# Kernel tuning notes

Hardware: AMD Instinct MI355X
Metric: run time of the kernel (lower is better)

The kernel has to match this reference:

```python
import jax, jax.numpy as jnp
import numpy as np

CHUNK = 32


def l2norm(x):
    return x * jax.lax.rsqrt(jnp.sum(x * x, -1, keepdims=True) + 1e-6)


def causal_dwconv(x, w):
    # x: (b, l, C), w: (C, 1, k) -- depthwise causal 1D conv (left pad k-1)
    k = w.shape[-1]
    xt = jnp.transpose(x, (0, 2, 1))
    xt = jnp.pad(xt, ((0, 0), (0, 0), (k - 1, 0)))
    y = jax.lax.conv_general_dilated(xt, w, (1,), 'VALID',
                                     dimension_numbers=('NCH', 'OIH', 'NCH'),
                                     feature_group_count=xt.shape[1])
    return jnp.transpose(y, (0, 2, 1))


def delta_rule_chunkwise(q, k, v, beta):
    # q,k: (b,h,L,dk), v: (b,h,L,dv), beta: (b,h,L). L must be divisible by CHUNK.
    b, h, L, dk = q.shape
    dv = v.shape[-1]
    n = L // CHUNK
    q = l2norm(q)
    k = l2norm(k)
    v = v * beta[..., None]
    kb = k * beta[..., None]
    resh = lambda t: t.reshape(b, h, n, CHUNK, t.shape[-1])
    q, k, v, kb = (resh(t) for t in (q, k, v, kb))
    strict = jnp.tril(jnp.ones((CHUNK, CHUNK), bool), -1)
    A = jnp.where(strict, -(kb @ jnp.swapaxes(k, -1, -2)), 0.0)
    eye = jnp.eye(CHUNK, dtype=A.dtype)
    # UT transform: the sequential forward-substitution loop computes T = (I - A)^{-1}
    T = jax.scipy.linalg.solve_triangular(eye - A, jnp.broadcast_to(eye, A.shape), lower=True)
    u = T @ v
    w = T @ kb
    incl = jnp.tril(jnp.ones((CHUNK, CHUNK), bool))  # lower incl. diag

    def step(S, xs):
        q_i, k_i, u_i, w_i = xs
        attn = jnp.where(incl, q_i @ jnp.swapaxes(k_i, -1, -2), 0.0)
        u_hat = u_i - w_i @ S
        o_i = q_i @ S + attn @ u_hat
        return S + jnp.swapaxes(k_i, -1, -2) @ u_hat, o_i

    xs = tuple(jnp.moveaxis(t, 2, 0) for t in (q, k, u, w))
    S0 = jnp.zeros((b, h, dk, dv), q.dtype)
    S, o = jax.lax.scan(step, S0, xs)
    o = jnp.moveaxis(o, 0, 2).reshape(b, h, L, dv)
    return o, S


def branch_stats(x):
    # per-head stats over the feature dim: mean, std(ddof=1), mean|x|, L2 norm
    m = jnp.mean(x, -1, keepdims=True)
    s = jnp.std(x, -1, keepdims=True, ddof=1)
    a = jnp.mean(jnp.abs(x), -1, keepdims=True)
    l = jnp.sqrt(jnp.sum(x * x, -1, keepdims=True))
    return jnp.concatenate([m, s, a, l], -1)


def reference(hidden_states, q_w, k_w, v_w, b_w, qc_w, kc_w, vc_w,
              fir_w1, fir_w3, fir_w7, fir_w31,
              mlp_w1, mlp_b1, mlp_w2, mlp_b2, gate_log_temp, onorm_w, o_w):
    B, L, D = hidden_states.shape
    H = gate_log_temp.shape[0]
    dk = q_w.shape[1] // H
    dv = v_w.shape[1] // H
    # projections + causal short conv + silu
    q = jax.nn.silu(causal_dwconv(hidden_states @ q_w, qc_w))
    k = jax.nn.silu(causal_dwconv(hidden_states @ k_w, kc_w))
    v = jax.nn.silu(causal_dwconv(hidden_states @ v_w, vc_w))
    q = q.reshape(B, L, H, dk)
    k = k.reshape(B, L, H, dk)
    v_direct = v.reshape(B, L, H, dv)
    beta = jax.nn.sigmoid(hidden_states @ b_w)  # (B,L,H)
    delta_out, _ = delta_rule_chunkwise(
        jnp.transpose(q, (0, 2, 1, 3)), jnp.transpose(k, (0, 2, 1, 3)),
        jnp.transpose(v_direct, (0, 2, 1, 3)), jnp.transpose(beta, (0, 2, 1)))
    delta_out = jnp.transpose(delta_out, (0, 2, 1, 3))  # (B,L,H,dv)
    # multi-scale depthwise FIR branches on v
    v_flat = v_direct.reshape(B, L, H * dv)
    firs = [causal_dwconv(v_flat, w).reshape(B, L, H, dv)
            for w in (fir_w1, fir_w3, fir_w7, fir_w31)]
    branches = firs + [delta_out, v_direct]  # num_streams = 6
    S = len(branches)
    stats = jnp.concatenate([branch_stats(x) for x in branches], -1)  # (B,L,H,S*4)
    gate_in = jnp.concatenate([hidden_states, stats.reshape(B, L, H * S * 4)], -1)
    hgate = jax.nn.gelu(gate_in @ mlp_w1 + mlp_b1, approximate=False)
    logits = (hgate @ mlp_w2 + mlp_b2).reshape(B, L, H, S)
    temp = jax.nn.softplus(gate_log_temp) + 0.5  # min_gate_temp = 0.5
    weights = jax.nn.softmax(logits / temp[None, None, :, None], axis=-1)
    fused = sum(weights[..., i, None] * br for i, br in enumerate(branches))
    # RMSNorm over head_v_dim (eps=1e-5)
    fused = fused * jax.lax.rsqrt(jnp.mean(fused * fused, -1, keepdims=True) + 1e-5) * onorm_w
    return fused.reshape(B, L, H * dv) @ o_w


def setup_inputs() -> dict:
    key = jax.random.key(0)
    B, L, D, H = 2, 2048, 1024, 4
    dk = dv = D // H
    S = 6
    ks = iter(jax.random.split(key, 32))
    nrm = lambda shape, s=0.02: jax.random.normal(next(ks), shape, jnp.float32) * s

    def fir(kw):
        # delta init (last tap = 1) plus small noise
        base = jnp.zeros((H * dv, 1, kw), jnp.float32).at[:, 0, -1].set(1.0)
        return base + nrm((H * dv, 1, kw))

    gate_in_dim = D + S * 4 * H  # 1120
    hgd = D * 2 // 2             # 1024
    b2 = np.zeros(H * S, np.float32)
    for h in range(H):
        b2[h * S + S - 1] = 2.0  # value_bias_init on direct-value stream
    return {
        'hidden_states': jax.random.normal(next(ks), (B, L, D), jnp.float32),
        'q_w': nrm((D, D)), 'k_w': nrm((D, D)), 'v_w': nrm((D, D)),
        'b_w': nrm((D, H)),
        'qc_w': nrm((D, 1, 4), 0.3), 'kc_w': nrm((D, 1, 4), 0.3), 'vc_w': nrm((D, 1, 4), 0.3),
        'fir_w1': fir(1), 'fir_w3': fir(3), 'fir_w7': fir(7), 'fir_w31': fir(31),
        'mlp_w1': nrm((gate_in_dim, hgd)), 'mlp_b1': jnp.zeros((hgd,), jnp.float32),
        'mlp_w2': nrm((hgd, H * S)), 'mlp_b2': jnp.asarray(b2),
        'gate_log_temp': jnp.zeros((H,), jnp.float32),
        'onorm_w': jnp.ones((dv,), jnp.float32),
        'o_w': nrm((D, D)),
    }
```

## Files before the change

### kernel.cpp

```cpp
#include <hip/hip_runtime.h>
#include <hip/hip_bf16.h>
#include <math.h>

#define B_ 2
#define L_ 2048
#define D_ 1024
#define H_ 4
#define NC 64

typedef unsigned short ushort_t;
typedef __bf16 bf16x8 __attribute__((ext_vector_type(8)));
typedef float f32x4 __attribute__((ext_vector_type(4)));
typedef ushort_t u16x8 __attribute__((ext_vector_type(8)));

__device__ __forceinline__ ushort_t f2bs(float f) {
    __hip_bfloat16 h = __float2bfloat16(f);
    ushort_t u;
    __builtin_memcpy(&u, &h, 2);
    return u;
}

__device__ __forceinline__ float wred(float v) {
    v += __shfl_down(v, 32);
    v += __shfl_down(v, 16);
    v += __shfl_down(v, 8);
    v += __shfl_down(v, 4);
    v += __shfl_down(v, 2);
    v += __shfl_down(v, 1);
    return v;
}

__device__ __forceinline__ void gload16(const void* g, void* l) {
    __builtin_amdgcn_global_load_lds((const __attribute__((address_space(1))) void*)g,
                                     (__attribute__((address_space(3))) void*)l, 16, 0, 0);
}

__global__ __launch_bounds__(256) void tcast_k(const float* __restrict__ W,
                                               ushort_t* __restrict__ WT, int K, int N) {
    __shared__ float tile[32 * 33];
    const int k0 = blockIdx.y << 5, n0 = blockIdx.x << 5;
    for (int e = threadIdx.x; e < 1024; e += 256)
        tile[(e >> 5) * 33 + (e & 31)] = W[(size_t)(k0 + (e >> 5)) * N + n0 + (e & 31)];
    __syncthreads();
    for (int e = threadIdx.x; e < 1024; e += 256)
        WT[(size_t)(n0 + (e >> 5)) * K + k0 + (e & 31)] = f2bs(tile[(e & 31) * 33 + (e >> 5)]);
}

__global__ __launch_bounds__(256) void cast_k(const float* __restrict__ x,
                                              ushort_t* __restrict__ y) {
    const int i = blockIdx.x * 256 + threadIdx.x;
    const float4 v = *(const float4*)&x[(size_t)i * 4];
    ushort4 p;
    p.x = f2bs(v.x); p.y = f2bs(v.y); p.z = f2bs(v.z); p.w = f2bs(v.w);
    *(ushort4*)&y[(size_t)i * 4] = p;
}

template <int ACT>
__global__ __launch_bounds__(256) void gemm_bf(const ushort_t* __restrict__ A,
                                               const ushort_t* __restrict__ Bt,
                                               const float* __restrict__ bias,
                                               float* __restrict__ C,
                                               int M, int N, int K) {
    __shared__ ushort_t As[128 * 32];
    __shared__ ushort_t Bs[128 * 32];
    const int t = threadIdx.x;
    const int wv = t >> 6, l = t & 63;
    const int m0 = blockIdx.y << 7, n0 = blockIdx.x << 7;
    const int wm = wv & 1, wn = wv >> 1;
    const int q4 = l >> 4, c16 = l & 15;
    f32x4 acc[4][4];
#pragma unroll
    for (int i = 0; i < 4; ++i)
#pragma unroll
        for (int j = 0; j < 4; ++j) {
            f32x4 z = {0.f, 0.f, 0.f, 0.f};
            acc[i][j] = z;
        }
    const int srow = (l >> 2);
    const int scol = (l & 3) << 3;
    for (int k0 = 0; k0 < K; k0 += 32) {
        __syncthreads();
#pragma unroll
        for (int si = 0; si < 2; ++si) {
            const int s = wv * 2 + si;
            gload16(&A[(size_t)(m0 + s * 16 + srow) * K + k0 + scol], &As[s * 512]);
            gload16(&Bt[(size_t)(n0 + s * 16 + srow) * K + k0 + scol], &Bs[s * 512]);
        }
        __syncthreads();
        bf16x8 af[4], bff[4];
#pragma unroll
        for (int mi = 0; mi < 4; ++mi)
            af[mi] = *(const bf16x8*)&As[(wm * 64 + mi * 16 + c16) * 32 + q4 * 8];
#pragma unroll
        for (int ni = 0; ni < 4; ++ni)
            bff[ni] = *(const bf16x8*)&Bs[(wn * 64 + ni * 16 + c16) * 32 + q4 * 8];
#pragma unroll
        for (int mi = 0; mi < 4; ++mi)
#pragma unroll
            for (int ni = 0; ni < 4; ++ni)
                acc[mi][ni] = __builtin_amdgcn_mfma_f32_16x16x32_bf16(af[mi], bff[ni],
                                                                     acc[mi][ni], 0, 0, 0);
    }
#pragma unroll
    for (int mi = 0; mi < 4; ++mi)
#pragma unroll
        for (int ni = 0; ni < 4; ++ni)
#pragma unroll
            for (int r = 0; r < 4; ++r) {
                const int row = m0 + wm * 64 + mi * 16 + q4 * 4 + r;
                const int col = n0 + wn * 64 + ni * 16 + c16;
                float v = acc[mi][ni][r];
                if (ACT == 1) {
                    v += bias[col];
                    v = 0.5f * v * (1.0f + erff(v * 0.70710678118654752f));
                }
                C[(size_t)row * N + col] = v;
            }
}

template <int DO_NORM, int EMIT_F32, int EMIT_BF>
__global__ __launch_bounds__(256) void convql_k(const float* __restrict__ X,
                                                const float* __restrict__ cw,
                                                float* __restrict__ Y,
                                                ushort_t* __restrict__ Ybf) {
    __shared__ float xs[35 * 256];
    const int bid = blockIdx.x;
    const int h = bid & 3, lt = (bid >> 2) & 63, b = bid >> 8;
    const int t = threadIdx.x;
    const int l0 = lt << 5;
    const int cg = (h << 8) | t;
    for (int e = t; e < 35 * 256; e += 256) {
        const int r = e >> 8, c = e & 255;
        const int gl = l0 + r - 3;
        xs[e] = (gl >= 0) ? X[((size_t)(b * L_) + gl) * 3072 + (h << 8) + c] : 0.f;
    }
    const float w0 = cw[cg * 4 + 0], w1 = cw[cg * 4 + 1];
    const float w2 = cw[cg * 4 + 2], w3 = cw[cg * 4 + 3];
    __syncthreads();
    float yr[32];
#pragma unroll
    for (int l = 0; l < 32; ++l) {
        const float a = xs[(l + 0) * 256 + t] * w0 + xs[(l + 1) * 256 + t] * w1 +
                        xs[(l + 2) * 256 + t] * w2 + xs[(l + 3) * 256 + t] * w3;
        yr[l] = a / (1.f + expf(-a));
    }
    if (DO_NORM) {
        __syncthreads();
#pragma unroll
        for (int l = 0; l < 32; ++l) xs[l * 256 + t] = yr[l];
        __syncthreads();
        const int wv = t >> 6, lane = t & 63;
#pragma unroll
        for (int ri = 0; ri < 8; ++ri) {
            const int r = wv * 8 + ri;
            float4 v = *(float4*)&xs[r * 256 + lane * 4];
            float ss = v.x * v.x + v.y * v.y + v.z * v.z + v.w * v.w;
            ss = wred(ss);
            ss = __shfl(ss, 0);
            const float s = rsqrtf(ss + 1e-6f);
            v.x *= s; v.y *= s; v.z *= s; v.w *= s;
            const size_t go = ((size_t)(b * L_) + l0 + r) * 1024 + (h << 8) + lane * 4;
            if (EMIT_F32) *(float4*)&Y[go] = v;
            if (EMIT_BF) {
                ushort4 p;
                p.x = f2bs(v.x); p.y = f2bs(v.y); p.z = f2bs(v.z); p.w = f2bs(v.w);
                *(ushort4*)&Ybf[go] = p;
            }
        }
    } else {
#pragma unroll
        for (int l = 0; l < 32; ++l)
            if (EMIT_F32) Y[((size_t)(b * L_) + l0 + l) * 1024 + cg] = yr[l];
    }
}

__global__ __launch_bounds__(256) void fir_k(const float* __restrict__ V,
                                             const float* __restrict__ w1w,
                                             const float* __restrict__ w3w,
                                             const float* __restrict__ w7w,
                                             const float* __restrict__ w31w,
                                             float* __restrict__ o1,
                                             float* __restrict__ o3,
                                             float* __restrict__ o7,
                                             float* __restrict__ o31) {
    __shared__ float xs[62 * 256];
    const int bid = blockIdx.x;
    const int h = bid & 3, lt = (bid >> 2) & 63, b = bid >> 8;
    const int t = threadIdx.x;
    const int l0 = lt << 5;
    const int cg = (h << 8) | t;
    for (int e = t; e < 62 * 256; e += 256) {
        const int r = e >> 8, c = e & 255;
        const int gl = l0 + r - 30;
        xs[e] = (gl >= 0) ? V[((size_t)(b * L_) + gl) * 1024 + (h << 8) + c] : 0.f;
    }
    float lw31[31], lw7[7], lw3[3];
#pragma unroll
    for (int j = 0; j < 31; ++j) lw31[j] = w31w[cg * 31 + j];
#pragma unroll
    for (int j = 0; j < 7; ++j) lw7[j] = w7w[cg * 7 + j];
#pragma unroll
    for (int j = 0; j < 3; ++j) lw3[j] = w3w[cg * 3 + j];
    const float lw1 = w1w[cg];
    __syncthreads();
    for (int l = 0; l < 32; ++l) {
        float a31 = 0.f, a7 = 0.f, a3 = 0.f, v = 0.f;
#pragma unroll
        for (int j = 0; j < 31; ++j) {
            v = xs[(l + j) * 256 + t];
            a31 += v * lw31[j];
            if (j >= 24) a7 += v * lw7[j - 24];
            if (j >= 28) a3 += v * lw3[j - 28];
        }
        const size_t go = ((size_t)(b * L_) + l0 + l) * 1024 + cg;
        o31[go] = a31;
        o7[go] = a7;
        o3[go] = a3;
        o1[go] = v * lw1;
    }
}

__global__ __launch_bounds__(64) void beta_k(const float* __restrict__ hs,
                                             const float* __restrict__ bw,
                                             float* __restrict__ beta,
                                             ushort_t* __restrict__ gin) {
    const int row = blockIdx.x;
    const int lane = threadIdx.x;
    float a0 = 0, a1 = 0, a2 = 0, a3 = 0;
    const float* hp = hs + (size_t)row * D_;
    ushort_t* gp = gin + (size_t)row * 1120;
    for (int c = lane; c < D_; c += 64) {
        const float x = hp[c];
        gp[c] = f2bs(x);
        a0 += x * bw[c * 4 + 0];
        a1 += x * bw[c * 4 + 1];
        a2 += x * bw[c * 4 + 2];
        a3 += x * bw[c * 4 + 3];
    }
    a0 = wred(a0); a1 = wred(a1); a2 = wred(a2); a3 = wred(a3);
    if (lane == 0) {
        float* o = beta + (size_t)row * 4;
        o[0] = 1.f / (1.f + expf(-a0));
        o[1] = 1.f / (1.f + expf(-a1));
        o[2] = 1.f / (1.f + expf(-a2));
        o[3] = 1.f / (1.f + expf(-a3));
    }
}

__global__ __launch_bounds__(256) void prep2_k(const ushort_t* __restrict__ qbf,
                                               const ushort_t* __restrict__ kbf,
                                               const float* __restrict__ vg,
                                               const float* __restrict__ beta,
                                               ushort_t* __restrict__ qfr,
                                               ushort_t* __restrict__ wfr,
                                               float* __restrict__ ufr,
                                               ushort_t* __restrict__ atfr,
                                               ushort_t* __restrict__ ktfr) {
    __shared__ ushort_t k_lds[32 * 264];
    __shared__ ushort_t kT_lds[256 * 32];
    __shared__ ushort_t vT_lds[256 * 32];
    __shared__ float Am[32 * 33];
    __shared__ float Tm[32 * 33];
    __shared__ ushort_t Tb[32 * 40];
    __shared__ ushort_t at_s[32 * 40];
    __shared__ float beta_s[32];
    const int bid = blockIdx.x;
    const int bh = bid >> 6, ci = bid & 63;
    const int b = bh >> 2, h = bh & 3;
    const int t = threadIdx.x;
    const int wv = t >> 6, lane = t & 63;
    const int mi = wv & 1, ni = wv >> 1;
    const int l16 = lane & 15, quad = lane >> 4;
    const size_t cb = (size_t)bid;
    const size_t grow = ((size_t)(b * L_ + ci * 32)) * 1024 + (h << 8);
    const f32x4 z4 = {0.f, 0.f, 0.f, 0.f};

    if (t < 32) beta_s[t] = beta[(size_t)(b * L_ + ci * 32 + t) * 4 + h];
#pragma unroll
    for (int j = 0; j < 4; ++j) {
        const int idx = j * 2048 + t * 8, r = idx >> 8, c = idx & 255;
        *(u16x8*)&k_lds[r * 264 + c] = *(const u16x8*)&kbf[grow + (size_t)r * 1024 + c];
    }
#pragma unroll
    for (int j = 0; j < 8; ++j) {
        const int e = j * 1024 + t * 4, r = e >> 8, c = e & 255;
        const float4 v4 = *(const float4*)&vg[grow + (size_t)r * 1024 + c];
        const float vv[4] = {v4.x, v4.y, v4.z, v4.w};
#pragma unroll
        for (int x = 0; x < 4; ++x) {
            const int cc = c + x;
            const int sp = (r >> 3) ^ ((cc >> 1) & 3);
            vT_lds[cc * 32 + sp * 8 + (r & 7)] = f2bs(vv[x]);
        }
    }
    f32x4 g = z4, atv = z4;
#pragma unroll
    for (int s = 0; s < 8; ++s) {
        const bf16x8 a =
            *(const bf16x8*)&kbf[grow + (size_t)(mi * 16 + l16) * 1024 + s * 32 + (quad << 3)];
        const bf16x8 bb =
            *(const bf16x8*)&kbf[grow + (size_t)(ni * 16 + l16) * 1024 + s * 32 + (quad << 3)];
        const bf16x8 qa =
            *(const bf16x8*)&qbf[grow + (size_t)(mi * 16 + l16) * 1024 + s * 32 + (quad << 3)];
        g = __builtin_amdgcn_mfma_f32_16x16x32_bf16(a, bb, g, 0, 0, 0);
        atv = __builtin_amdgcn_mfma_f32_16x16x32_bf16(qa, bb, atv, 0, 0, 0);
        if (ni == 0) *(bf16x8*)&qfr[((cb * 2 + mi) * 8 + s) * 512 + lane * 8] = qa;
    }
    __syncthreads();
#pragma unroll
    for (int r = 0; r < 4; ++r) {
        const int row = mi * 16 + (quad << 2) + r;
        const int col = ni * 16 + l16;
        Am[row * 33 + col] = (col < row) ? -beta_s[row] * g[r] : 0.f;
        Tm[row * 33 + col] = (row == col) ? 1.f : 0.f;
        at_s[row * 40 + col] = (col <= row) ? f2bs(atv[r]) : (ushort_t)0;
    }
#pragma unroll
    for (int j = 0; j < 8; ++j) {
        const int e = j * 1024 + t * 4, r = e >> 8, c = e & 255;
#pragma unroll
        for (int x = 0; x < 4; ++x) {
            const int cc = c + x;
            const int sp = (r >> 3) ^ ((cc >> 1) & 3);
            kT_lds[cc * 32 + sp * 8 + (r & 7)] = k_lds[r * 264 + cc];
        }
    }
    __syncthreads();
    if (wv < 2) {
        const u16x8 av = *(const u16x8*)&at_s[(wv * 16 + l16) * 40 + (quad << 3)];
        *(u16x8*)&atfr[(cb * 2 + wv) * 512 + lane * 8] = av;
    }
#pragma unroll
    for (int j2 = 0; j2 < 4; ++j2) {
        const int tc = wv * 4 + j2;
        const int c = tc * 16 + l16;
        const int sp = quad ^ ((c >> 1) & 3);
        *(u16x8*)&ktfr[(cb * 16 + tc) * 512 + lane * 8] = *(const u16x8*)&kT_lds[c * 32 + sp * 8];
    }
    for (int i = 1; i < 32; ++i) {
        if (t < 32) {
            float s = 0.f;
            for (int j = 0; j < i; ++j) s += Am[i * 33 + j] * Tm[j * 33 + t];
            Tm[i * 33 + t] += s;
        }
        __syncthreads();
    }
#pragma unroll
    for (int j = 0; j < 4; ++j) {
        const int e = j * 256 + t, i = e >> 5, jj = e & 31;
        Tb[i * 40 + jj] = f2bs(Tm[i * 33 + jj] * beta_s[jj]);
    }
    __syncthreads();
    const bf16x8 tf = *(const bf16x8*)&Tb[(mi * 16 + l16) * 40 + (quad << 3)];
#pragma unroll
    for (int j = 0; j < 8; ++j) {
        const int nt = ni * 8 + j;
        const int d = (nt << 4) + l16;
        const int sp = quad ^ ((d >> 1) & 3);
        const bf16x8 kb = *(const bf16x8*)&kT_lds[d * 32 + (sp << 3)];
        const bf16x8 vb = *(const bf16x8*)&vT_lds[d * 32 + (sp << 3)];
        const f32x4 wacc = __builtin_amdgcn_mfma_f32_16x16x32_bf16(tf, kb, z4, 0, 0, 0);
        const f32x4 uacc = __builtin_amdgcn_mfma_f32_16x16x32_bf16(tf, vb, z4, 0, 0, 0);
        *(float4*)&ufr[((cb * 16 + nt) * 2 + mi) * 256 + lane * 4] =
            make_float4(uacc[0], uacc[1], uacc[2], uacc[3]);
#pragma unroll
        for (int r = 0; r < 4; ++r) {
            const int row = mi * 16 + (quad << 2) + r;
            k_lds[row * 264 + d] = f2bs(wacc[r]);
        }
    }
    __syncthreads();
    if (wv < 2) {
#pragma unroll
        for (int s = 0; s < 8; ++s) {
            const u16x8 wv8 = *(const u16x8*)&k_lds[(wv * 16 + l16) * 264 + s * 32 + (quad << 3)];
            *(u16x8*)&wfr[((cb * 2 + wv) * 8 + s) * 512 + lane * 8] = wv8;
        }
    }
}

__global__ __launch_bounds__(64, 1) void scan7_k(const ushort_t* __restrict__ qfr,
                                                 const ushort_t* __restrict__ wfr,
                                                 const float* __restrict__ ufr,
                                                 const ushort_t* __restrict__ atfr,
                                                 const ushort_t* __restrict__ ktfr,
                                                 float* __restrict__ dlt) {
    __shared__ ushort_t qstg[2][16 * 512];
    __shared__ ushort_t wstg[2][16 * 512];
    __shared__ ushort_t atstg[2][2 * 512];
    __shared__ float ustg[2][2 * 256];
    __shared__ ushort_t Sm[8 * 512];
    __shared__ ushort_t uhL[512];
    const int l = threadIdx.x;
    const int q = l >> 4, c = l & 15;
    const int bh = blockIdx.x & 7, tile = blockIdx.x >> 3;
    const int b = bh >> 2, h = bh & 3;

    const int4 z16 = {0, 0, 0, 0};
#pragma unroll
    for (int e = 0; e < 8; ++e) *(int4*)&Sm[(e * 64 + l) * 8] = z16;

    f32x4 Sacc[16];
#pragma unroll
    for (int tc = 0; tc < 16; ++tc) {
        f32x4 z = {0.f, 0.f, 0.f, 0.f};
        Sacc[tc] = z;
    }

    auto stage = [&](int ci, int p) {
        const size_t cb = (size_t)(bh * NC + ci);
        const ushort_t* qsrc = qfr + cb * (16 * 512);
        const ushort_t* wsrc = wfr + cb * (16 * 512);
#pragma unroll
        for (int f = 0; f < 16; ++f) gload16(&qsrc[f * 512 + l * 8], &qstg[p][f * 512]);
#pragma unroll
        for (int f = 0; f < 16; ++f) gload16(&wsrc[f * 512 + l * 8], &wstg[p][f * 512]);
#pragma unroll
        for (int hf = 0; hf < 2; ++hf)
            gload16(&atfr[(cb * 2 + hf) * 512 + l * 8], &atstg[p][hf * 512]);
#pragma unroll
        for (int hf = 0; hf < 2; ++hf)
            gload16(&ufr[((cb * 16 + tile) * 2 + hf) * 256 + l * 4], &ustg[p][hf * 256]);
    };

    stage(0, 0);
    asm volatile("s_waitcnt vmcnt(0)" ::: "memory");
    __builtin_amdgcn_sched_barrier(0);

    for (int ci = 0; ci < NC; ++ci) {
        const int p = ci & 1;
        asm volatile("s_waitcnt vmcnt(8)" ::: "memory");
        __builtin_amdgcn_sched_barrier(0);
        const size_t cb = (size_t)(bh * NC + ci);
        bf16x8 ktf[16];
        const ushort_t* ksrc = ktfr + cb * (16 * 512);
#pragma unroll
        for (int tc = 0; tc < 16; ++tc)
            ktf[tc] = *(const bf16x8*)&ksrc[tc * 512 + l * 8];
        if (ci + 1 < NC) stage(ci + 1, p ^ 1);

        f32x4 aw0[2], aw1[2], oq0[2], oq1[2];
#pragma unroll
        for (int hf = 0; hf < 2; ++hf) {
            f32x4 z = {0.f, 0.f, 0.f, 0.f};
            aw0[hf] = z; aw1[hf] = z; oq0[hf] = z; oq1[hf] = z;
        }
#pragma unroll
        for (int s = 0; s < 8; ++s) {
            const bf16x8 Sb = *(const bf16x8*)&Sm[(s * 64 + l) * 8];
            const bf16x8 w0 = *(const bf16x8*)&wstg[p][(0 * 8 + s) * 512 + l * 8];
            const bf16x8 w1 = *(const bf16x8*)&wstg[p][(1 * 8 + s) * 512 + l * 8];
            const bf16x8 q0 = *(const bf16x8*)&qstg[p][(0 * 8 + s) * 512 + l * 8];
            const bf16x8 q1 = *(const bf16x8*)&qstg[p][(1 * 8 + s) * 512 + l * 8];
            if (s & 1) {
                aw1[0] = __builtin_amdgcn_mfma_f32_16x16x32_bf16(w0, Sb, aw1[0], 0, 0, 0);
                aw1[1] = __builtin_amdgcn_mfma_f32_16x16x32_bf16(w1, Sb, aw1[1], 0, 0, 0);
                oq1[0] = __builtin_amdgcn_mfma_f32_16x16x32_bf16(q0, Sb, oq1[0], 0, 0, 0);
                oq1[1] = __builtin_amdgcn_mfma_f32_16x16x32_bf16(q1, Sb, oq1[1], 0, 0, 0);
            } else {
                aw0[0] = __builtin_amdgcn_mfma_f32_16x16x32_bf16(w0, Sb, aw0[0], 0, 0, 0);
                aw0[1] = __builtin_amdgcn_mfma_f32_16x16x32_bf16(w1, Sb, aw0[1], 0, 0, 0);
                oq0[0] = __builtin_amdgcn_mfma_f32_16x16x32_bf16(q0, Sb, oq0[0], 0, 0, 0);
                oq0[1] = __builtin_amdgcn_mfma_f32_16x16x32_bf16(q1, Sb, oq0[1], 0, 0, 0);
            }
        }
#pragma unroll
        for (int hf = 0; hf < 2; ++hf) {
            const float4 uv = *(const float4*)&ustg[p][hf * 256 + l * 4];
            ushort4 up;
            up.x = f2bs(uv.x - aw0[hf][0] - aw1[hf][0]);
            up.y = f2bs(uv.y - aw0[hf][1] - aw1[hf][1]);
            up.z = f2bs(uv.z - aw0[hf][2] - aw1[hf][2]);
            up.w = f2bs(uv.w - aw0[hf][3] - aw1[hf][3]);
            *(ushort4*)&uhL[((2 * hf + (q >> 1)) * 16 + c) * 8 + (q & 1) * 4] = up;
        }
        const bf16x8 uhB = *(const bf16x8*)&uhL[l * 8];
#pragma unroll
        for (int tc = 0; tc < 16; ++tc) {
            Sacc[tc] = __builtin_amdgcn_mfma_f32_16x16x32_bf16(ktf[tc], uhB, Sacc[tc], 0, 0, 0);
            ushort4 pk;
            pk.x = f2bs(Sacc[tc][0]);
            pk.y = f2bs(Sacc[tc][1]);
            pk.z = f2bs(Sacc[tc][2]);
            pk.w = f2bs(Sacc[tc][3]);
            *(ushort4*)&Sm[(((tc >> 1) * 64) + ((tc & 1) * 2 + (q >> 1)) * 16 + c) * 8 +
                           (q & 1) * 4] = pk;
        }
        const bf16x8 at0 = *(const bf16x8*)&atstg[p][0 * 512 + l * 8];
        const bf16x8 at1 = *(const bf16x8*)&atstg[p][1 * 512 + l * 8];
        oq0[0] = __builtin_amdgcn_mfma_f32_16x16x32_bf16(at0, uhB, oq0[0], 0, 0, 0);
        oq0[1] = __builtin_amdgcn_mfma_f32_16x16x32_bf16(at1, uhB, oq0[1], 0, 0, 0);
        const size_t gbase = ((size_t)(b * L_ + ci * 32)) * 1024 + (h << 8) + (tile << 4) + c;
#pragma unroll
        for (int hf = 0; hf < 2; ++hf)
#pragma unroll
            for (int r = 0; r < 4; ++r)
                dlt[gbase + (size_t)(hf * 16 + (q << 2) + r) * 1024] = oq0[hf][r] + oq1[hf][r];
    }
}

__global__ __launch_bounds__(64) void stats_k(const float* __restrict__ f1,
                                              const float* __restrict__ f3,
                                              const float* __restrict__ f7,
                                              const float* __restrict__ f31,
                                              const float* __restrict__ dl,
                                              const float* __restrict__ vv,
                                              ushort_t* __restrict__ gin) {
    const int row = blockIdx.x;
    const int lane = threadIdx.x;
    const float* ptrs[6] = {f1, f3, f7, f31, dl, vv};
    const size_t base = (size_t)row * 256;
    ushort_t* gp = gin + (size_t)(row >> 2) * 1120 + 1024 + (row & 3) * 24;
    for (int br = 0; br < 6; ++br) {
        const float4 x = *(const float4*)&ptrs[br][base + lane * 4];
        float s1 = x.x + x.y + x.z + x.w;
        float s2 = x.x * x.x + x.y * x.y + x.z * x.z + x.w * x.w;
        float sa = fabsf(x.x) + fabsf(x.y) + fabsf(x.z) + fabsf(x.w);
        s1 = wred(s1); s2 = wred(s2); sa = wred(sa);
        if (lane == 0) {
            const float m = s1 / 256.f;
            float var = (s2 - 256.f * m * m) / 255.f;
            if (var < 0.f) var = 0.f;
            gp[br * 4 + 0] = f2bs(m);
            gp[br * 4 + 1] = f2bs(sqrtf(var));
            gp[br * 4 + 2] = f2bs(sa / 256.f);
            gp[br * 4 + 3] = f2bs(sqrtf(s2));
        }
    }
}

__global__ __launch_bounds__(256) void wts_k(const float* __restrict__ hg,
                                             const float* __restrict__ w2,
                                             const float* __restrict__ b2,
                                             const float* __restrict__ glt,
                                             float* __restrict__ wts) {
    const int row = blockIdx.x;
    const int h = threadIdx.x >> 6, lane = threadIdx.x & 63;
    float hv[16];
    const float* hp = hg + (size_t)row * 1024;
#pragma unroll
    for (int ii = 0; ii < 16; ++ii) hv[ii] = hp[lane + 64 * ii];
    float lg[6];
#pragma unroll
    for (int s = 0; s < 6; ++s) {
        const int j = h * 6 + s;
        float acc = 0.f;
#pragma unroll
        for (int ii = 0; ii < 16; ++ii) acc += hv[ii] * w2[(size_t)(lane + 64 * ii) * 24 + j];
        lg[s] = wred(acc);
    }
    if (lane == 0) {
        const float temp = log1pf(expf(glt[h])) + 0.5f;
        float mx = -1e30f;
#pragma unroll
        for (int s = 0; s < 6; ++s) {
            lg[s] = (lg[s] + b2[h * 6 + s]) / temp;
            mx = fmaxf(mx, lg[s]);
        }
        float se = 0.f;
#pragma unroll
        for (int s = 0; s < 6; ++s) {
            lg[s] = expf(lg[s] - mx);
            se += lg[s];
        }
        float* o = &wts[(size_t)row * 24 + h * 6];
        const float inv = 1.f / se;
#pragma unroll
        for (int s = 0; s < 6; ++s) o[s] = lg[s] * inv;
    }
}

__global__ __launch_bounds__(1024) void fuse_k(const float* __restrict__ f1,
                                               const float* __restrict__ f3,
                                               const float* __restrict__ f7,
                                               const float* __restrict__ f31,
                                               const float* __restrict__ dl,
                                               const float* __restrict__ vv,
                                               const float* __restrict__ wts,
                                               const float* __restrict__ onw,
                                               ushort_t* __restrict__ fused) {
    __shared__ float wloc[24];
    __shared__ float psum[16];
    const int row = blockIdx.x, t = threadIdx.x;
    if (t < 24) wloc[t] = wts[(size_t)row * 24 + t];
    __syncthreads();
    const int h = t >> 8, dd = t & 255;
    const size_t idx = (size_t)row * 1024 + t;
    const float* ptrs[6] = {f1, f3, f7, f31, dl, vv};
    float f = 0.f;
#pragma unroll
    for (int br = 0; br < 6; ++br) f += wloc[h * 6 + br] * ptrs[br][idx];
    float ss = wred(f * f);
    const int wave = t >> 6;
    if ((t & 63) == 0) psum[wave] = ss;
    __syncthreads();
    const float tot = psum[h * 4 + 0] + psum[h * 4 + 1] + psum[h * 4 + 2] + psum[h * 4 + 3];
    const float scale = rsqrtf(tot / 256.f + 1e-5f);
    fused[idx] = f2bs(f * scale * onw[dd]);
}

extern "C" void kernel_launch(void* const* d_in, const int* in_sizes, int n_in,
                              void* d_out, int out_size, void* d_ws, size_t ws_size,
                              hipStream_t stream) {
    const float* hs   = (const float*)d_in[0];
    const float* q_w  = (const float*)d_in[1];
    const float* k_w  = (const float*)d_in[2];
    const float* v_w  = (const float*)d_in[3];
    const float* b_w  = (const float*)d_in[4];
    const float* qc_w = (const float*)d_in[5];
    const float* kc_w = (const float*)d_in[6];
    const float* vc_w = (const float*)d_in[7];
    const float* f1w  = (const float*)d_in[8];
    const float* f3w  = (const float*)d_in[9];
    const float* f7w  = (const float*)d_in[10];
    const float* f31w = (const float*)d_in[11];
    const float* w1   = (const float*)d_in[12];
    const float* b1   = (const float*)d_in[13];
    const float* w2   = (const float*)d_in[14];
    const float* b2   = (const float*)d_in[15];
    const float* glt  = (const float*)d_in[16];
    const float* onw  = (const float*)d_in[17];
    const float* o_w  = (const float*)d_in[18];
    float* out = (float*)d_out;

    const size_t SZ = (size_t)B_ * L_ * D_;
    float* qlin = (float*)d_ws;
    float* klin = qlin + SZ;
    float* vlin = klin + SZ;
    float* qbuf = vlin + SZ;
    float* kbuf = qbuf + SZ;
    float* vbuf = kbuf + SZ;
    float* f31b = vbuf + SZ;
    float* wb   = f31b + SZ;
    float* ub   = wb + SZ;
    float* dlt  = ub + SZ;
    float* beta = dlt + SZ;
    float* attn = beta + (size_t)B_ * L_ * H_;
    float* f1b = qlin;
    float* f3b = klin;
    float* f7b = vlin;
    float* hgate = kbuf;
    float* qkv = qlin;
    float* wts = attn + (size_t)B_ * H_ * NC * 1024;

    ushort_t* hs_bf = (ushort_t*)dlt;
    ushort_t* qwT = (ushort_t*)f31b;
    ushort_t* kwT = (ushort_t*)f31b + 1048576;
    ushort_t* vwT = (ushort_t*)f31b + 2097152;
    ushort_t* qbf = (ushort_t*)f31b + 3145728;
    ushort_t* kbf = (ushort_t*)kbuf;
    ushort_t* gin_bf = (ushort_t*)qbuf;
    ushort_t* w1T = (ushort_t*)(wb + 2359296);
    ushort_t* owT = (ushort_t*)ub;
    ushort_t* fused_bf = (ushort_t*)kbuf;
    ushort_t* ktfr = (ushort_t*)klin;
    ushort_t* qfr = (ushort_t*)klin + SZ;
    ushort_t* wfr = (ushort_t*)wb;
    float* ufr = ub;
    ushort_t* atfr = (ushort_t*)attn;

    const int M = B_ * L_;

    tcast_k<<<dim3(32, 32), 256, 0, stream>>>(q_w, qwT, 1024, 1024);
    tcast_k<<<dim3(32, 32), 256, 0, stream>>>(k_w, kwT, 1024, 1024);
    tcast_k<<<dim3(32, 32), 256, 0, stream>>>(v_w, vwT, 1024, 1024);
    cast_k<<<4096, 256, 0, stream>>>(hs, hs_bf);
    gemm_bf<0><<<dim3(24, 32), 256, 0, stream>>>(hs_bf, qwT, nullptr, qkv, M, 3072, 1024);
    beta_k<<<M, 64, 0, stream>>>(hs, b_w, beta, gin_bf);
    convql_k<1, 0, 1><<<512, 256, 0, stream>>>(qkv + 0,    qc_w, nullptr, qbf);
    convql_k<1, 0, 1><<<512, 256, 0, stream>>>(qkv + 1024, kc_w, nullptr, kbf);
    convql_k<0, 1, 0><<<512, 256, 0, stream>>>(qkv + 2048, vc_w, vbuf, nullptr);
    prep2_k<<<B_ * H_ * NC, 256, 0, stream>>>(qbf, kbf, vbuf, beta, qfr, wfr, ufr, atfr, ktfr);
    scan7_k<<<128, 64, 0, stream>>>(qfr, wfr, ufr, atfr, ktfr, dlt);
    fir_k<<<512, 256, 0, stream>>>(vbuf, f1w, f3w, f7w, f31w, f1b, f3b, f7b, f31b);
    stats_k<<<M * H_, 64, 0, stream>>>(f1b, f3b, f7b, f31b, dlt, vbuf, gin_bf);
    tcast_k<<<dim3(32, 35), 256, 0, stream>>>(w1, w1T, 1120, 1024);
    gemm_bf<1><<<dim3(8, 32), 256, 0, stream>>>(gin_bf, w1T, b1, hgate, M, 1024, 1120);
    wts_k<<<M, 256, 0, stream>>>(hgate, w2, b2, glt, wts);
    fuse_k<<<M, 1024, 0, stream>>>(f1b, f3b, f7b, f31b, dlt, vbuf, wts, onw, fused_bf);
    tcast_k<<<dim3(32, 32), 256, 0, stream>>>(o_w, owT, 1024, 1024);
    gemm_bf<0><<<dim3(8, 32), 256, 0, stream>>>(fused_bf, owT, nullptr, out, M, 1024, 1024);
}
```

Measured before the change: 585.0 us.

## Keep scan state in registers by re-laying MFMA fragments to avoid LDS round-trips

The prep kernel now writes the q, attn, k^T and w fragments in a permuted k-order, with each lane's 8 elements drawn as two 4-element halves 16 apart. This lets the MFMA output of S (bf16-packed) and u_hat feed straight back as B operands from registers, so the scan no longer stages S and u_hat through shared memory between MFMAs. The scan also prefetches the next chunk's k^T fragments into double-buffered registers and unrolls two chunks per iteration, and it drops the split even/odd accumulators. The cost is much higher register pressure in a serial, one-wave-per-block kernel, plus a strict requirement that the permuted layout stays consistent across both kernels.

```diff
diff --git a/kernel.cpp b/kernel.cpp
--- a/kernel.cpp
+++ b/kernel.cpp
@@ -12,6 +12,8 @@
 typedef __bf16 bf16x8 __attribute__((ext_vector_type(8)));
 typedef float f32x4 __attribute__((ext_vector_type(4)));
 typedef ushort_t u16x8 __attribute__((ext_vector_type(8)));
+typedef short s16x8 __attribute__((ext_vector_type(8)));
+typedef short s16x4 __attribute__((ext_vector_type(4)));
 
 __device__ __forceinline__ ushort_t f2bs(float f) {
     __hip_bfloat16 h = __float2bfloat16(f);
@@ -33,6 +35,16 @@
 __device__ __forceinline__ void gload16(const void* g, void* l) {
     __builtin_amdgcn_global_load_lds((const __attribute__((address_space(1))) void*)g,
                                      (__attribute__((address_space(3))) void*)l, 16, 0, 0);
+}
+
+__device__ __forceinline__ s16x4 pack4(float a, float b, float c, float d) {
+    ushort4 u;
+    u.x = f2bs(a); u.y = f2bs(b); u.z = f2bs(c); u.w = f2bs(d);
+    return __builtin_bit_cast(s16x4, u);
+}
+__device__ __forceinline__ bf16x8 cat8(s16x4 lo, s16x4 hi) {
+    s16x8 r = __builtin_shufflevector(lo, hi, 0, 1, 2, 3, 4, 5, 6, 7);
+    return __builtin_bit_cast(bf16x8, r);
 }
 
 __global__ __launch_bounds__(256) void tcast_k(const float* __restrict__ W,
@@ -304,7 +316,14 @@
             *(const bf16x8*)&qbf[grow + (size_t)(mi * 16 + l16) * 1024 + s * 32 + (quad << 3)];
         g = __builtin_amdgcn_mfma_f32_16x16x32_bf16(a, bb, g, 0, 0, 0);
         atv = __builtin_amdgcn_mfma_f32_16x16x32_bf16(qa, bb, atv, 0, 0, 0);
-        if (ni == 0) *(bf16x8*)&qfr[((cb * 2 + mi) * 8 + s) * 512 + lane * 8] = qa;
+        if (ni == 0) {
+            const size_t ga = grow + (size_t)(mi * 16 + l16) * 1024 + s * 32 + (quad << 2);
+            const ushort4 q0 = *(const ushort4*)&qbf[ga];
+            const ushort4 q1 = *(const ushort4*)&qbf[ga + 16];
+            ushort_t* qd = &qfr[((cb * 2 + mi) * 8 + s) * 512 + lane * 8];
+            *(ushort4*)qd = q0;
+            *(ushort4*)(qd + 4) = q1;
+        }
     }
     __syncthreads();
 #pragma unroll
@@ -327,15 +346,24 @@
     }
     __syncthreads();
     if (wv < 2) {
-        const u16x8 av = *(const u16x8*)&at_s[(wv * 16 + l16) * 40 + (quad << 3)];
-        *(u16x8*)&atfr[(cb * 2 + wv) * 512 + lane * 8] = av;
+        const int ra = (wv * 16 + l16) * 40 + (quad << 2);
+        const ushort4 a0 = *(const ushort4*)&at_s[ra];
+        const ushort4 a1 = *(const ushort4*)&at_s[ra + 16];
+        ushort_t* ad = &atfr[(cb * 2 + wv) * 512 + lane * 8];
+        *(ushort4*)ad = a0;
+        *(ushort4*)(ad + 4) = a1;
     }
 #pragma unroll
     for (int j2 = 0; j2 < 4; ++j2) {
         const int tc = wv * 4 + j2;
-        const int c = tc * 16 + l16;
-        const int sp = quad ^ ((c >> 1) & 3);
-        *(u16x8*)&ktfr[(cb * 16 + tc) * 512 + lane * 8] = *(const u16x8*)&kT_lds[c * 32 + sp * 8];
+        const int d = tc * 16 + l16;
+        const int x = (d >> 1) & 3;
+        const int base = d * 32 + ((quad & 1) << 2);
+        const ushort4 k0 = *(const ushort4*)&kT_lds[base + ((((quad >> 1) + 0) ^ x) << 3)];
+        const ushort4 k1 = *(const ushort4*)&kT_lds[base + ((((quad >> 1) + 2) ^ x) << 3)];
+        ushort_t* kd = &ktfr[(cb * 16 + tc) * 512 + lane * 8];
+        *(ushort4*)kd = k0;
+        *(ushort4*)(kd + 4) = k1;
     }
     for (int i = 1; i < 32; ++i) {
         if (t < 32) {
@@ -372,14 +400,18 @@
     __syncthreads();
     if (wv < 2) {
 #pragma unroll
-        for (int s = 0; s < 8; ++s) {
-            const u16x8 wv8 = *(const u16x8*)&k_lds[(wv * 16 + l16) * 264 + s * 32 + (quad << 3)];
-            *(u16x8*)&wfr[((cb * 2 + wv) * 8 + s) * 512 + lane * 8] = wv8;
-        }
-    }
-}
-
-__global__ __launch_bounds__(64, 1) void scan7_k(const ushort_t* __restrict__ qfr,
+        for (int sp = 0; sp < 8; ++sp) {
+            const int rb = (wv * 16 + l16) * 264 + sp * 32 + (quad << 2);
+            const ushort4 w0 = *(const ushort4*)&k_lds[rb];
+            const ushort4 w1 = *(const ushort4*)&k_lds[rb + 16];
+            ushort_t* wd = &wfr[((cb * 2 + wv) * 8 + sp) * 512 + lane * 8];
+            *(ushort4*)wd = w0;
+            *(ushort4*)(wd + 4) = w1;
+        }
+    }
+}
+
+__global__ __launch_bounds__(64, 1) void scan9_k(const ushort_t* __restrict__ qfr,
                                                  const ushort_t* __restrict__ wfr,
                                                  const float* __restrict__ ufr,
                                                  const ushort_t* __restrict__ atfr,
@@ -389,23 +421,21 @@
     __shared__ ushort_t wstg[2][16 * 512];
     __shared__ ushort_t atstg[2][2 * 512];
     __shared__ float ustg[2][2 * 256];
-    __shared__ ushort_t Sm[8 * 512];
-    __shared__ ushort_t uhL[512];
     const int l = threadIdx.x;
-    const int q = l >> 4, c = l & 15;
+    const int qd = l >> 4, c = l & 15;
     const int bh = blockIdx.x & 7, tile = blockIdx.x >> 3;
     const int b = bh >> 2, h = bh & 3;
 
-    const int4 z16 = {0, 0, 0, 0};
-#pragma unroll
-    for (int e = 0; e < 8; ++e) *(int4*)&Sm[(e * 64 + l) * 8] = z16;
-
     f32x4 Sacc[16];
+    s16x4 SB[16];
 #pragma unroll
     for (int tc = 0; tc < 16; ++tc) {
         f32x4 z = {0.f, 0.f, 0.f, 0.f};
         Sacc[tc] = z;
-    }
+        s16x4 zs = {0, 0, 0, 0};
+        SB[tc] = zs;
+    }
+    s16x8 ktA[16], ktB[16];
 
     auto stage = [&](int ci, int p) {
         const size_t cb = (size_t)(bh * NC + ci);
@@ -423,80 +453,68 @@
             gload16(&ufr[((cb * 16 + tile) * 2 + hf) * 256 + l * 4], &ustg[p][hf * 256]);
     };
 
+    {
+        const ushort_t* ksrc = ktfr + (size_t)(bh * NC) * (16 * 512);
+#pragma unroll
+        for (int tc = 0; tc < 16; ++tc) ktA[tc] = *(const s16x8*)&ksrc[tc * 512 + l * 8];
+    }
     stage(0, 0);
     asm volatile("s_waitcnt vmcnt(0)" ::: "memory");
     __builtin_amdgcn_sched_barrier(0);
 
-    for (int ci = 0; ci < NC; ++ci) {
-        const int p = ci & 1;
-        asm volatile("s_waitcnt vmcnt(8)" ::: "memory");
-        __builtin_amdgcn_sched_barrier(0);
-        const size_t cb = (size_t)(bh * NC + ci);
-        bf16x8 ktf[16];
-        const ushort_t* ksrc = ktfr + cb * (16 * 512);
-#pragma unroll
-        for (int tc = 0; tc < 16; ++tc)
-            ktf[tc] = *(const bf16x8*)&ksrc[tc * 512 + l * 8];
-        if (ci + 1 < NC) stage(ci + 1, p ^ 1);
-
-        f32x4 aw0[2], aw1[2], oq0[2], oq1[2];
-#pragma unroll
-        for (int hf = 0; hf < 2; ++hf) {
-            f32x4 z = {0.f, 0.f, 0.f, 0.f};
-            aw0[hf] = z; aw1[hf] = z; oq0[hf] = z; oq1[hf] = z;
-        }
-#pragma unroll
-        for (int s = 0; s < 8; ++s) {
-            const bf16x8 Sb = *(const bf16x8*)&Sm[(s * 64 + l) * 8];
-            const bf16x8 w0 = *(const bf16x8*)&wstg[p][(0 * 8 + s) * 512 + l * 8];
-            const bf16x8 w1 = *(const bf16x8*)&wstg[p][(1 * 8 + s) * 512 + l * 8];
-            const bf16x8 q0 = *(const bf16x8*)&qstg[p][(0 * 8 + s) * 512 + l * 8];
-            const bf16x8 q1 = *(const bf16x8*)&qstg[p][(1 * 8 + s) * 512 + l * 8];
-            if (s & 1) {
-                aw1[0] = __builtin_amdgcn_mfma_f32_16x16x32_bf16(w0, Sb, aw1[0], 0, 0, 0);
-                aw1[1] = __builtin_amdgcn_mfma_f32_16x16x32_bf16(w1, Sb, aw1[1], 0, 0, 0);
-                oq1[0] = __builtin_amdgcn_mfma_f32_16x16x32_bf16(q0, Sb, oq1[0], 0, 0, 0);
-                oq1[1] = __builtin_amdgcn_mfma_f32_16x16x32_bf16(q1, Sb, oq1[1], 0, 0, 0);
-            } else {
-                aw0[0] = __builtin_amdgcn_mfma_f32_16x16x32_bf16(w0, Sb, aw0[0], 0, 0, 0);
-                aw0[1] = __builtin_amdgcn_mfma_f32_16x16x32_bf16(w1, Sb, aw0[1], 0, 0, 0);
-                oq0[0] = __builtin_amdgcn_mfma_f32_16x16x32_bf16(q0, Sb, oq0[0], 0, 0, 0);
-                oq0[1] = __builtin_amdgcn_mfma_f32_16x16x32_bf16(q1, Sb, oq0[1], 0, 0, 0);
-            }
-        }
-#pragma unroll
-        for (int hf = 0; hf < 2; ++hf) {
-            const float4 uv = *(const float4*)&ustg[p][hf * 256 + l * 4];
-            ushort4 up;
-            up.x = f2bs(uv.x - aw0[hf][0] - aw1[hf][0]);
-            up.y = f2bs(uv.y - aw0[hf][1] - aw1[hf][1]);
-            up.z = f2bs(uv.z - aw0[hf][2] - aw1[hf][2]);
-            up.w = f2bs(uv.w - aw0[hf][3] - aw1[hf][3]);
-            *(ushort4*)&uhL[((2 * hf + (q >> 1)) * 16 + c) * 8 + (q & 1) * 4] = up;
-        }
-        const bf16x8 uhB = *(const bf16x8*)&uhL[l * 8];
-#pragma unroll
-        for (int tc = 0; tc < 16; ++tc) {
-            Sacc[tc] = __builtin_amdgcn_mfma_f32_16x16x32_bf16(ktf[tc], uhB, Sacc[tc], 0, 0, 0);
-            ushort4 pk;
-            pk.x = f2bs(Sacc[tc][0]);
-            pk.y = f2bs(Sacc[tc][1]);
-            pk.z = f2bs(Sacc[tc][2]);
-            pk.w = f2bs(Sacc[tc][3]);
-            *(ushort4*)&Sm[(((tc >> 1) * 64) + ((tc & 1) * 2 + (q >> 1)) * 16 + c) * 8 +
-                           (q & 1) * 4] = pk;
-        }
-        const bf16x8 at0 = *(const bf16x8*)&atstg[p][0 * 512 + l * 8];
-        const bf16x8 at1 = *(const bf16x8*)&atstg[p][1 * 512 + l * 8];
-        oq0[0] = __builtin_amdgcn_mfma_f32_16x16x32_bf16(at0, uhB, oq0[0], 0, 0, 0);
-        oq0[1] = __builtin_amdgcn_mfma_f32_16x16x32_bf16(at1, uhB, oq0[1], 0, 0, 0);
-        const size_t gbase = ((size_t)(b * L_ + ci * 32)) * 1024 + (h << 8) + (tile << 4) + c;
-#pragma unroll
-        for (int hf = 0; hf < 2; ++hf)
-#pragma unroll
-            for (int r = 0; r < 4; ++r)
-                dlt[gbase + (size_t)(hf * 16 + (q << 2) + r) * 1024] = oq0[hf][r] + oq1[hf][r];
-    }
+#define SC_BODY(CI, P, KT, KTN)                                                              \
+    {                                                                                        \
+        asm volatile("s_waitcnt vmcnt(8)" ::: "memory");                                     \
+        __builtin_amdgcn_sched_barrier(0);                                                   \
+        if ((CI) + 1 < NC) {                                                                 \
+            const ushort_t* ksrc = ktfr + (size_t)(bh * NC + (CI) + 1) * (16 * 512);         \
+            _Pragma("unroll") for (int tc = 0; tc < 16; ++tc)                                \
+                KTN[tc] = *(const s16x8*)&ksrc[tc * 512 + l * 8];                            \
+            stage((CI) + 1, (P) ^ 1);                                                        \
+        }                                                                                    \
+        f32x4 aw[2], oq[2];                                                                  \
+        _Pragma("unroll") for (int hf = 0; hf < 2; ++hf) {                                   \
+            f32x4 z = {0.f, 0.f, 0.f, 0.f};                                                  \
+            aw[hf] = z;                                                                      \
+            oq[hf] = z;                                                                      \
+        }                                                                                    \
+        _Pragma("unroll") for (int sp = 0; sp < 8; ++sp) {                                   \
+            const bf16x8 Sop = cat8(SB[2 * sp + 0], SB[2 * sp + 1]);                         \
+            _Pragma("unroll") for (int hf = 0; hf < 2; ++hf) {                               \
+                const bf16x8 wv8 = *(const bf16x8*)&wstg[P][(hf * 8 + sp) * 512 + l * 8];    \
+                const bf16x8 qv8 = *(const bf16x8*)&qstg[P][(hf * 8 + sp) * 512 + l * 8];    \
+                aw[hf] = __builtin_amdgcn_mfma_f32_16x16x32_bf16(wv8, Sop, aw[hf], 0, 0, 0); \
+                oq[hf] = __builtin_amdgcn_mfma_f32_16x16x32_bf16(qv8, Sop, oq[hf], 0, 0, 0); \
+            }                                                                                \
+        }                                                                                    \
+        s16x4 uhB[2];                                                                        \
+        _Pragma("unroll") for (int hf = 0; hf < 2; ++hf) {                                   \
+            const float4 uv = *(const float4*)&ustg[P][hf * 256 + l * 4];                    \
+            uhB[hf] = pack4(uv.x - aw[hf][0], uv.y - aw[hf][1],                              \
+                            uv.z - aw[hf][2], uv.w - aw[hf][3]);                             \
+        }                                                                                    \
+        const bf16x8 Uop = cat8(uhB[0], uhB[1]);                                             \
+        _Pragma("unroll") for (int tc = 0; tc < 16; ++tc) {                                  \
+            Sacc[tc] = __builtin_amdgcn_mfma_f32_16x16x32_bf16(                              \
+                __builtin_bit_cast(bf16x8, KT[tc]), Uop, Sacc[tc], 0, 0, 0);                 \
+            SB[tc] = pack4(Sacc[tc][0], Sacc[tc][1], Sacc[tc][2], Sacc[tc][3]);              \
+        }                                                                                    \
+        _Pragma("unroll") for (int hf = 0; hf < 2; ++hf) {                                   \
+            const bf16x8 av = *(const bf16x8*)&atstg[P][hf * 512 + l * 8];                   \
+            oq[hf] = __builtin_amdgcn_mfma_f32_16x16x32_bf16(av, Uop, oq[hf], 0, 0, 0);      \
+        }                                                                                    \
+        const size_t gbase =                                                                 \
+            ((size_t)(b * L_ + (CI) * 32)) * 1024 + (h << 8) + (tile << 4) + c;              \
+        _Pragma("unroll") for (int hf = 0; hf < 2; ++hf)                                     \
+            _Pragma("unroll") for (int r = 0; r < 4; ++r)                                    \
+                dlt[gbase + (size_t)(hf * 16 + (qd << 2) + r) * 1024] = oq[hf][r];           \
+    }
+
+    for (int ci = 0; ci < NC; ci += 2) {
+        SC_BODY(ci, 0, ktA, ktB)
+        SC_BODY(ci + 1, 1, ktB, ktA)
+    }
+#undef SC_BODY
 }
 
 __global__ __launch_bounds__(64) void stats_k(const float* __restrict__ f1,
@@ -671,7 +689,7 @@
     convql_k<1, 0, 1><<<512, 256, 0, stream>>>(qkv + 1024, kc_w, nullptr, kbf);
     convql_k<0, 1, 0><<<512, 256, 0, stream>>>(qkv + 2048, vc_w, vbuf, nullptr);
     prep2_k<<<B_ * H_ * NC, 256, 0, stream>>>(qbf, kbf, vbuf, beta, qfr, wfr, ufr, atfr, ktfr);
-    scan7_k<<<128, 64, 0, stream>>>(qfr, wfr, ufr, atfr, ktfr, dlt);
+    scan9_k<<<128, 64, 0, stream>>>(qfr, wfr, ufr, atfr, ktfr, dlt);
     fir_k<<<512, 256, 0, stream>>>(vbuf, f1w, f3w, f7w, f31w, f1b, f3b, f7b, f31b);
     stats_k<<<M * H_, 64, 0, stream>>>(f1b, f3b, f7b, f31b, dlt, vbuf, gin_bf);
     tcast_k<<<dim3(32, 35), 256, 0, stream>>>(w1, w1T, 1120, 1024);
```

After: 564.9 us. 1.04x faster.
